# Optimization experiments

Measured on AMD Instinct MI355X. Metric: run time of the kernel, lower is better.

## Reference

```python
import jax, jax.numpy as jnp
import numpy as np
import math

B, N, E, H = 2, 2048, 1024, 16
K = E // H  # head dim = 64


def setup_inputs() -> dict:
    key = jax.random.key(0)
    ks = jax.random.split(key, 9)
    s = 0.02
    return {
        "x": jax.random.normal(ks[0], (B, N, E), jnp.float32),
        "Wq": jax.random.normal(ks[1], (E, E), jnp.float32) * s,
        "bq": jax.random.normal(ks[2], (E,), jnp.float32) * s,
        "Wk": jax.random.normal(ks[3], (E, E), jnp.float32) * s,
        "bk": jax.random.normal(ks[4], (E,), jnp.float32) * s,
        "Wv": jax.random.normal(ks[5], (E, E), jnp.float32) * s,
        "bv": jax.random.normal(ks[6], (E,), jnp.float32) * s,
        "Wp": jax.random.normal(ks[7], (E, E), jnp.float32) * s,
        "bp": jax.random.normal(ks[8], (E,), jnp.float32) * s,
    }


def _split_heads(t):
    # torch: t.transpose(-1,-2).view(b, H, K, N)  -> (B, H, K, N)
    return t.transpose(0, 2, 1).reshape(t.shape[0], H, K, t.shape[1])


def reference(x, Wq, bq, Wk, bk, Wv, bv, Wp, bp):
    b, n, _ = x.shape
    q = _split_heads(x @ Wq.T + bq)  # (B,H,K,N)
    k = _split_heads(x @ Wk.T + bk)
    v = _split_heads(x @ Wv.T + bv)
    # NOTE: module divides by sqrt(query.size(1)) == sqrt(num_heads), not sqrt(head_dim)
    ctx = jnp.einsum('bhkn,bhkm->bhmn', q, k) / math.sqrt(H)  # (B,H,m=key,n=query)
    mask = jnp.triu(jnp.ones((n, n), dtype=bool), 1)  # True where n(query) > m(key)
    ctx = jnp.where(mask[None, None], -jnp.inf, ctx)
    # faithful to source: softmax over last axis (the query axis n)
    ctx = jax.nn.softmax(ctx, axis=-1)
    out = jnp.einsum('bhmn,bhvm->bhvn', ctx, v)  # (B,H,K,N)
    out = out.reshape(b, E, n).transpose(0, 2, 1)  # (B,N,E)
    return out @ Wp.T + bp
```

## Files before the change

### kernel.cpp

```cpp
#include <hip/hip_runtime.h>
#include <hip/hip_bf16.h>

typedef __hip_bfloat16 bf16;
typedef __attribute__((ext_vector_type(8))) short bf16x8;
typedef __attribute__((ext_vector_type(4))) float f32x4;
typedef __attribute__((ext_vector_type(4))) short s16x4;

constexpr int B_ = 2, N_ = 2048, E_ = 1024, H_ = 16, KD_ = 64;
constexpr int M_ = B_ * N_;
constexpr float SCALE = 0.25f * 1.44269504088896f;

#define MFMA16(A, Bf, C) __builtin_amdgcn_mfma_f32_16x16x32_bf16(A, Bf, C, 0, 0, 0)
#define SBAR() do { __builtin_amdgcn_s_barrier(); __builtin_amdgcn_sched_barrier(0); } while (0)
#define WAITCNT(s) asm volatile("s_waitcnt " s ::: "memory")
#define SETPRIO(p) __builtin_amdgcn_s_setprio(p)

typedef const __attribute__((address_space(1))) void* gptr_t;
typedef __attribute__((address_space(3))) void* sptr_t;

__device__ inline short bf16bits(float f) {
  bf16 h = __float2bfloat16(f);
  short s;
  __builtin_memcpy(&s, &h, 2);
  return s;
}
__device__ inline float bf16f(short s) {
  bf16 h;
  __builtin_memcpy(&h, &s, 2);
  return __bfloat162float(h);
}

template <int NROWS, int NTHR>
__device__ inline void stageT(const bf16* __restrict__ base, int stride_elems,
                              char* lds) {
  const int t = threadIdx.x;
#pragma unroll
  for (int i = 0; i < NROWS * 128 / (NTHR * 16); i++) {
    int L = i * NTHR * 16 + t * 16;
    int row = L >> 7;
    int slot = ((L >> 4) & 7) ^ (row & 7);
    const bf16* src = base + (size_t)row * stride_elems + slot * 8;
    __builtin_amdgcn_global_load_lds((gptr_t)(const void*)src,
                                     (sptr_t)(void*)(lds + L), 16, 0, 0);
  }
}

__device__ inline bf16x8 frag_ld(const char* lds, int row, int ks) {
  const int g = (threadIdx.x >> 4) & 3;
  const int off = (ks * 64 + g * 16) ^ ((row & 7) << 4);
  return *(const bf16x8*)(lds + row * 128 + off);
}

__global__ __launch_bounds__(256) void cvt_all(
    const float* __restrict__ x, const float* __restrict__ wq,
    const float* __restrict__ wk, const float* __restrict__ wv,
    const float* __restrict__ wp, bf16* __restrict__ dst) {
  const size_t XN = (size_t)M_ * E_;
  const size_t WN = (size_t)E_ * E_;
  size_t i = ((size_t)blockIdx.x * 256 + threadIdx.x) * 4;
  const float* src;
  size_t off;
  if (i < XN) { src = x; off = i; }
  else if (i < XN + WN) { src = wq; off = i - XN; }
  else if (i < XN + 2 * WN) { src = wk; off = i - XN - WN; }
  else if (i < XN + 3 * WN) { src = wv; off = i - XN - 2 * WN; }
  else { src = wp; off = i - XN - 3 * WN; }
  float4 v = *(const float4*)(src + off);
  s16x4 o;
  o[0] = bf16bits(v.x); o[1] = bf16bits(v.y);
  o[2] = bf16bits(v.z); o[3] = bf16bits(v.w);
  *(s16x4*)(dst + i) = o;
}

__global__ __launch_bounds__(256) void gemm_qkv(
    const bf16* __restrict__ A, const bf16* __restrict__ Wb,
    const float* __restrict__ bq, const float* __restrict__ bk,
    const float* __restrict__ bv, bf16* __restrict__ Qhd,
    bf16* __restrict__ Khd, bf16* __restrict__ Vtd) {
  __shared__ char Asm[16384];
  __shared__ char Bsm[16384];
  const int t = threadIdx.x, lane = t & 63, w = t >> 6;
  const int wr = w >> 1, wc = w & 1;
  const int c = lane & 15, g = lane >> 4;
  const int row0 = blockIdx.y * 128, col0 = blockIdx.x * 128;
  f32x4 acc[4][4] = {};

  for (int k0 = 0; k0 < E_; k0 += 64) {
    stageT<64, 256>(A + (size_t)row0 * E_ + k0, E_, Asm);
    stageT<64, 256>(A + (size_t)(row0 + 64) * E_ + k0, E_, Asm + 8192);
    stageT<64, 256>(Wb + (size_t)col0 * E_ + k0, E_, Bsm);
    stageT<64, 256>(Wb + (size_t)(col0 + 64) * E_ + k0, E_, Bsm + 8192);
    __syncthreads();
#pragma unroll
    for (int ks = 0; ks < 2; ks++) {
      bf16x8 af[4], bfr[4];
#pragma unroll
      for (int mi = 0; mi < 4; mi++) af[mi] = frag_ld(Asm, wr * 64 + mi * 16 + c, ks);
#pragma unroll
      for (int ni = 0; ni < 4; ni++) bfr[ni] = frag_ld(Bsm, wc * 64 + ni * 16 + c, ks);
#pragma unroll
      for (int mi = 0; mi < 4; mi++)
#pragma unroll
        for (int ni = 0; ni < 4; ni++)
          acc[mi][ni] = MFMA16(af[mi], bfr[ni], acc[mi][ni]);
    }
    __syncthreads();
  }

  const int sel = col0 >> 10;
  const float* biasp = sel == 0 ? bq : sel == 1 ? bk : bv;
  bf16* outp = sel == 0 ? Qhd : sel == 1 ? Khd : Vtd;
#pragma unroll
  for (int mi = 0; mi < 4; mi++) {
#pragma unroll
    for (int ni = 0; ni < 4; ni++) {
      const int row = row0 + wr * 64 + mi * 16 + g * 4;
      const int col = col0 + wc * 64 + ni * 16 + c;
      const int ccol = col & 1023, h = ccol >> 6, kd = ccol & 63;
      const float bvf = biasp[ccol];
      if (sel < 2) {
        const float scl = (sel == 1) ? SCALE : 1.0f;
#pragma unroll
        for (int r = 0; r < 4; r++) {
          const int rr = row + r, b = rr >> 11, n = rr & (N_ - 1);
          outp[(((size_t)(b * H_ + h)) * N_ + n) * KD_ + kd] =
              __float2bfloat16((acc[mi][ni][r] + bvf) * scl);
        }
      } else {
        const int b = row >> 11, n = row & (N_ - 1);
        s16x4 o;
#pragma unroll
        for (int r = 0; r < 4; r++) o[r] = bf16bits(acc[mi][ni][r] + bvf);
        *(s16x4*)&outp[(((size_t)(b * H_ + h)) * KD_ + kd) * N_ + n] = o;
      }
    }
  }
}

__global__ __launch_bounds__(256) void gemm_proj(
    const bf16* __restrict__ A, const bf16* __restrict__ Wb,
    const float* __restrict__ bias, float* __restrict__ outf) {
  __shared__ char Asm[16384];
  __shared__ char Bsm[16384];
  const int t = threadIdx.x, lane = t & 63, w = t >> 6;
  const int wr = w >> 1, wc = w & 1;
  const int c = lane & 15, g = lane >> 4;
  const int row0 = blockIdx.y * 128, col0 = blockIdx.x * 128;
  f32x4 acc[4][4] = {};

  for (int k0 = 0; k0 < E_; k0 += 64) {
    stageT<64, 256>(A + (size_t)row0 * E_ + k0, E_, Asm);
    stageT<64, 256>(A + (size_t)(row0 + 64) * E_ + k0, E_, Asm + 8192);
    stageT<64, 256>(Wb + (size_t)col0 * E_ + k0, E_, Bsm);
    stageT<64, 256>(Wb + (size_t)(col0 + 64) * E_ + k0, E_, Bsm + 8192);
    __syncthreads();
#pragma unroll
    for (int ks = 0; ks < 2; ks++) {
      bf16x8 af[4], bfr[4];
#pragma unroll
      for (int mi = 0; mi < 4; mi++) af[mi] = frag_ld(Asm, wr * 64 + mi * 16 + c, ks);
#pragma unroll
      for (int ni = 0; ni < 4; ni++) bfr[ni] = frag_ld(Bsm, wc * 64 + ni * 16 + c, ks);
#pragma unroll
      for (int mi = 0; mi < 4; mi++)
#pragma unroll
        for (int ni = 0; ni < 4; ni++)
          acc[mi][ni] = MFMA16(af[mi], bfr[ni], acc[mi][ni]);
    }
    __syncthreads();
  }

#pragma unroll
  for (int mi = 0; mi < 4; mi++) {
#pragma unroll
    for (int ni = 0; ni < 4; ni++) {
      const int row = row0 + wr * 64 + mi * 16 + g * 4;
      const int col = col0 + wc * 64 + ni * 16 + c;
      const float bvf = bias[col];
#pragma unroll
      for (int r = 0; r < 4; r++)
        outf[(size_t)(row + r) * E_ + col] = acc[mi][ni][r] + bvf;
    }
  }
}

__device__ inline void swz_bid(int& qx, int& bh) {
  const int bid = blockIdx.y * 16 + blockIdx.x;
  const int w = (bid & 7) * 64 + (bid >> 3);
  qx = w & 15;
  bh = w >> 4;
}

__global__ __launch_bounds__(512, 4) void phaseA(
    const bf16* __restrict__ Kh, const bf16* __restrict__ Qh,
    bf16* __restrict__ Vt) {
  __shared__ char Ksm[8192];
  __shared__ char Qsm[2][16384];
  __shared__ float rbuf[2][64];
  const int t = threadIdx.x, lane = t & 63, w = t >> 6;
  const int c = lane & 15, g = (lane >> 4);
  const int wm = w & 3, wn = w >> 2;
  int bx, bh;
  swz_bid(bx, bh);
  const bf16* Kb = Kh + (size_t)bh * N_ * KD_;
  const bf16* Qb = Qh + (size_t)bh * N_ * KD_;
  bf16* Vtb = Vt + (size_t)bh * KD_ * N_;

#pragma unroll 1
  for (int seg = 0; seg < 2; seg++) {
    const int mb = seg ? (31 - bx) : bx;
    const int m0 = mb * 64;
    const int ntE = mb >> 1;

    WAITCNT("lgkmcnt(0)");
    SBAR();
    stageT<64, 512>(Kb + (size_t)m0 * KD_, KD_, Ksm);
    stageT<128, 512>(Qb, KD_, Qsm[0]);
    WAITCNT("vmcnt(2)");
    SBAR();
    bf16x8 af0 = frag_ld(Ksm, wm * 16 + c, 0);
    bf16x8 af1 = frag_ld(Ksm, wm * 16 + c, 1);
    float sm[4] = {};

#pragma unroll 1
    for (int nt = 0; nt <= ntE; nt++) {
      WAITCNT("vmcnt(0) lgkmcnt(0)");
      SBAR();
      if (nt + 1 <= ntE)
        stageT<128, 512>(Qb + (size_t)(nt + 1) * 128 * KD_, KD_,
                         Qsm[(nt + 1) & 1]);
      const char* qs = Qsm[nt & 1];
      if (nt < ntE) {
#pragma unroll
        for (int nf = 0; nf < 4; nf++) {
          const int ni = wn * 4 + nf;
          bf16x8 b0 = frag_ld(qs, ni * 16 + c, 0);
          bf16x8 b1 = frag_ld(qs, ni * 16 + c, 1);
          SETPRIO(1);
          f32x4 sv = {0.f, 0.f, 0.f, 0.f};
          sv = MFMA16(af0, b0, sv);
          sv = MFMA16(af1, b1, sv);
          SETPRIO(0);
#pragma unroll
          for (int r = 0; r < 4; r++) sm[r] += exp2f(sv[r]);
        }
      } else {
        const int mg = m0 + wm * 16 + g * 4;
#pragma unroll
        for (int nf = 0; nf < 4; nf++) {
          const int ni = wn * 4 + nf;
          bf16x8 b0 = frag_ld(qs, ni * 16 + c, 0);
          bf16x8 b1 = frag_ld(qs, ni * 16 + c, 1);
          SETPRIO(1);
          f32x4 sv = {0.f, 0.f, 0.f, 0.f};
          sv = MFMA16(af0, b0, sv);
          sv = MFMA16(af1, b1, sv);
          SETPRIO(0);
          const int ng = nt * 128 + ni * 16 + c;
#pragma unroll
          for (int r = 0; r < 4; r++) {
            float e = exp2f(sv[r]);
            sm[r] += (ng <= mg + r) ? e : 0.f;
          }
        }
      }
    }

#pragma unroll
    for (int r = 0; r < 4; r++) {
      float v = sm[r];
#pragma unroll
      for (int d = 1; d < 16; d <<= 1) v += __shfl_xor(v, d, 64);
      if (c == 0) rbuf[wn][wm * 16 + g * 4 + r] = v;
    }
    WAITCNT("lgkmcnt(0)");
    SBAR();
    {
      const int kd = t >> 3, mc = (t & 7) * 8;
      bf16* p = Vtb + (size_t)kd * N_ + m0 + mc;
      bf16x8 v = *(const bf16x8*)p;
      bf16x8 o;
#pragma unroll
      for (int j = 0; j < 8; j++) {
        const float inv = 1.0f / (rbuf[0][mc + j] + rbuf[1][mc + j]);
        o[j] = bf16bits(bf16f(v[j]) * inv);
      }
      *(bf16x8*)p = o;
    }
  }
}

__global__ __launch_bounds__(512, 4) void phaseB(
    const bf16* __restrict__ Qh, const bf16* __restrict__ Kh,
    const bf16* __restrict__ Vt, bf16* __restrict__ attn) {
  __shared__ char Ksm[2][8192];
  __shared__ char Vsm[2][8192];
  __shared__ char Psm[8192];
  const int t = threadIdx.x, lane = t & 63, w = t >> 6;
  const int c = lane & 15, g = lane >> 4;
  const int wm = w & 3, wn = w >> 2;
  int bx, bh;
  swz_bid(bx, bh);
  const int b = bh >> 4, h = bh & 15;
  const int NT = N_ / 64;
  const bf16* Qb = Qh + (size_t)bh * N_ * KD_;
  const bf16* Kb = Kh + (size_t)bh * N_ * KD_;
  const bf16* Vb = Vt + (size_t)bh * KD_ * N_;

#pragma unroll 1
  for (int seg = 0; seg < 2; seg++) {
    const int qt = seg ? (31 - bx) : bx;
    const int n0 = qt * 64, mt0 = qt;

    WAITCNT("lgkmcnt(0)");
    SBAR();
    stageT<64, 512>(Qb + (size_t)n0 * KD_, KD_, Psm);
    stageT<64, 512>(Kb + (size_t)mt0 * 64 * KD_, KD_, Ksm[mt0 & 1]);
    stageT<64, 512>(Vb + mt0 * 64, N_, Vsm[mt0 & 1]);
    WAITCNT("vmcnt(2)");
    SBAR();
    bf16x8 qf[2][2];
#pragma unroll
    for (int ni = 0; ni < 2; ni++) {
      qf[ni][0] = frag_ld(Psm, wn * 32 + ni * 16 + c, 0);
      qf[ni][1] = frag_ld(Psm, wn * 32 + ni * 16 + c, 1);
    }
    f32x4 out[2] = {};

#pragma unroll 1
    for (int mt = mt0; mt < NT; mt++) {
      WAITCNT("vmcnt(0) lgkmcnt(0)");
      SBAR();
      if (mt + 1 < NT) {
        stageT<64, 512>(Kb + (size_t)(mt + 1) * 64 * KD_, KD_, Ksm[(mt + 1) & 1]);
        stageT<64, 512>(Vb + (mt + 1) * 64, N_, Vsm[(mt + 1) & 1]);
      }
      const char* ksm = Ksm[mt & 1];
      bf16x8 kf0 = frag_ld(ksm, wm * 16 + c, 0);
      bf16x8 kf1 = frag_ld(ksm, wm * 16 + c, 1);
      SETPRIO(1);
      f32x4 sv[2];
#pragma unroll
      for (int ni = 0; ni < 2; ni++) {
        f32x4 z = {0.f, 0.f, 0.f, 0.f};
        z = MFMA16(kf0, qf[ni][0], z);
        z = MFMA16(kf1, qf[ni][1], z);
        sv[ni] = z;
      }
      SETPRIO(0);
      const bool diag = (mt == mt0);
      const int ml = wm * 16 + g * 4;
#pragma unroll
      for (int ni = 0; ni < 2; ni++) {
        const int nl = wn * 32 + ni * 16 + c;
        s16x4 p;
#pragma unroll
        for (int r = 0; r < 4; r++) {
          float val = exp2f(sv[ni][r]);
          if (diag && nl > (ml + r)) val = 0.f;
          p[r] = bf16bits(val);
        }
        const int off = nl * 128 + ((wm * 32 + g * 8) ^ ((nl & 7) << 4));
        *(s16x4*)(Psm + off) = p;
      }
      WAITCNT("lgkmcnt(0)");
      SBAR();
      const char* vsm = Vsm[mt & 1];
      bf16x8 pa0 = frag_ld(Psm, wm * 16 + c, 0);
      bf16x8 pa1 = frag_ld(Psm, wm * 16 + c, 1);
      SETPRIO(1);
#pragma unroll
      for (int ni = 0; ni < 2; ni++) {
        const int kdrow = wn * 32 + ni * 16 + c;
        bf16x8 v0 = frag_ld(vsm, kdrow, 0);
        bf16x8 v1 = frag_ld(vsm, kdrow, 1);
        out[ni] = MFMA16(pa0, v0, out[ni]);
        out[ni] = MFMA16(pa1, v1, out[ni]);
      }
      SETPRIO(0);
    }

#pragma unroll
    for (int ni = 0; ni < 2; ni++) {
#pragma unroll
      for (int r = 0; r < 4; r++) {
        const int n = n0 + wm * 16 + g * 4 + r;
        const int kd = wn * 32 + ni * 16 + c;
        attn[((size_t)(b * N_ + n)) * E_ + h * 64 + kd] =
            __float2bfloat16(out[ni][r]);
      }
    }
  }
}

extern "C" void kernel_launch(void* const* d_in, const int* in_sizes, int n_in,
                              void* d_out, int out_size, void* d_ws, size_t ws_size,
                              hipStream_t stream) {
  (void)in_sizes; (void)n_in; (void)out_size; (void)ws_size;
  const float* x  = (const float*)d_in[0];
  const float* Wq = (const float*)d_in[1];
  const float* bq = (const float*)d_in[2];
  const float* Wk = (const float*)d_in[3];
  const float* bk = (const float*)d_in[4];
  const float* Wv = (const float*)d_in[5];
  const float* bv = (const float*)d_in[6];
  const float* Wp = (const float*)d_in[7];
  const float* bp = (const float*)d_in[8];
  float* out = (float*)d_out;

  const size_t XN = (size_t)M_ * E_;
  const size_t WN = (size_t)E_ * E_;
  const size_t HN = (size_t)B_ * H_ * N_ * KD_;

  bf16* xb   = (bf16*)d_ws;
  bf16* wqkv = xb + XN;
  bf16* wpb  = wqkv + 3 * WN;
  bf16* Qhd  = wpb + WN;
  bf16* Khd  = Qhd + HN;
  bf16* Vtd  = Khd + HN;
  bf16* attn = xb;

  cvt_all<<<dim3(8192), 256, 0, stream>>>(x, Wq, Wk, Wv, Wp, xb);

  gemm_qkv<<<dim3(24, 32), 256, 0, stream>>>(xb, wqkv, bq, bk, bv,
                                             Qhd, Khd, Vtd);

  phaseA<<<dim3(16, B_ * H_), 512, 0, stream>>>(Khd, Qhd, Vtd);
  phaseB<<<dim3(16, B_ * H_), 512, 0, stream>>>(Qhd, Khd, Vtd, attn);

  gemm_proj<<<dim3(8, 32), 256, 0, stream>>>(attn, wpb, bp, out);
}
```

Baseline: 136.2 us.

## Widen attention key tile to 128 to halve loop iterations and barriers

Measured after the change: 137.8 us. About the same (+1.2%).

```diff
diff --git a/kernel.cpp b/kernel.cpp
--- a/kernel.cpp
+++ b/kernel.cpp
@@ -45,10 +45,31 @@
   }
 }
 
+template <int NROWS, int NTHR>
+__device__ inline void stage256(const bf16* __restrict__ base, int stride_elems,
+                                char* lds) {
+  const int t = threadIdx.x;
+#pragma unroll
+  for (int i = 0; i < NROWS * 256 / (NTHR * 16); i++) {
+    int L = i * NTHR * 16 + t * 16;
+    int row = L >> 8;
+    int slot = ((L >> 4) & 15) ^ (row & 15);
+    const bf16* src = base + (size_t)row * stride_elems + slot * 8;
+    __builtin_amdgcn_global_load_lds((gptr_t)(const void*)src,
+                                     (sptr_t)(void*)(lds + L), 16, 0, 0);
+  }
+}
+
 __device__ inline bf16x8 frag_ld(const char* lds, int row, int ks) {
   const int g = (threadIdx.x >> 4) & 3;
   const int off = (ks * 64 + g * 16) ^ ((row & 7) << 4);
   return *(const bf16x8*)(lds + row * 128 + off);
+}
+
+__device__ inline bf16x8 frag_ld256(const char* lds, int row, int ks) {
+  const int g = (threadIdx.x >> 4) & 3;
+  const int off = (ks * 64 + g * 16) ^ ((row & 15) << 4);
+  return *(const bf16x8*)(lds + row * 256 + off);
 }
 
 __global__ __launch_bounds__(256) void cvt_all(
@@ -293,16 +314,15 @@
 __global__ __launch_bounds__(512, 4) void phaseB(
     const bf16* __restrict__ Qh, const bf16* __restrict__ Kh,
     const bf16* __restrict__ Vt, bf16* __restrict__ attn) {
-  __shared__ char Ksm[2][8192];
-  __shared__ char Vsm[2][8192];
-  __shared__ char Psm[8192];
+  __shared__ char Ksm[2][16384];
+  __shared__ char Vsm[2][16384];
+  __shared__ char Psm[16384];
   const int t = threadIdx.x, lane = t & 63, w = t >> 6;
   const int c = lane & 15, g = lane >> 4;
-  const int wm = w & 3, wn = w >> 2;
   int bx, bh;
   swz_bid(bx, bh);
   const int b = bh >> 4, h = bh & 15;
-  const int NT = N_ / 64;
+  const int NT = N_ / 128;
   const bf16* Qb = Qh + (size_t)bh * N_ * KD_;
   const bf16* Kb = Kh + (size_t)bh * N_ * KD_;
   const bf16* Vb = Vt + (size_t)bh * KD_ * N_;
@@ -310,20 +330,20 @@
 #pragma unroll 1
   for (int seg = 0; seg < 2; seg++) {
     const int qt = seg ? (31 - bx) : bx;
-    const int n0 = qt * 64, mt0 = qt;
+    const int n0 = qt * 64, mt0 = qt >> 1;
 
     WAITCNT("lgkmcnt(0)");
     SBAR();
     stageT<64, 512>(Qb + (size_t)n0 * KD_, KD_, Psm);
-    stageT<64, 512>(Kb + (size_t)mt0 * 64 * KD_, KD_, Ksm[mt0 & 1]);
-    stageT<64, 512>(Vb + mt0 * 64, N_, Vsm[mt0 & 1]);
-    WAITCNT("vmcnt(2)");
+    stageT<128, 512>(Kb + (size_t)mt0 * 128 * KD_, KD_, Ksm[mt0 & 1]);
+    stage256<64, 512>(Vb + mt0 * 128, N_, Vsm[mt0 & 1]);
+    WAITCNT("vmcnt(4)");
     SBAR();
-    bf16x8 qf[2][2];
-#pragma unroll
-    for (int ni = 0; ni < 2; ni++) {
-      qf[ni][0] = frag_ld(Psm, wn * 32 + ni * 16 + c, 0);
-      qf[ni][1] = frag_ld(Psm, wn * 32 + ni * 16 + c, 1);
+    bf16x8 qf[4][2];
+#pragma unroll
+    for (int ni = 0; ni < 4; ni++) {
+      qf[ni][0] = frag_ld(Psm, ni * 16 + c, 0);
+      qf[ni][1] = frag_ld(Psm, ni * 16 + c, 1);
     }
     f32x4 out[2] = {};
 
@@ -332,16 +352,17 @@
       WAITCNT("vmcnt(0) lgkmcnt(0)");
       SBAR();
       if (mt + 1 < NT) {
-        stageT<64, 512>(Kb + (size_t)(mt + 1) * 64 * KD_, KD_, Ksm[(mt + 1) & 1]);
-        stageT<64, 512>(Vb + (mt + 1) * 64, N_, Vsm[(mt + 1) & 1]);
+        stageT<128, 512>(Kb + (size_t)(mt + 1) * 128 * KD_, KD_,
+                         Ksm[(mt + 1) & 1]);
+        stage256<64, 512>(Vb + (mt + 1) * 128, N_, Vsm[(mt + 1) & 1]);
       }
       const char* ksm = Ksm[mt & 1];
-      bf16x8 kf0 = frag_ld(ksm, wm * 16 + c, 0);
-      bf16x8 kf1 = frag_ld(ksm, wm * 16 + c, 1);
+      bf16x8 kf0 = frag_ld(ksm, w * 16 + c, 0);
+      bf16x8 kf1 = frag_ld(ksm, w * 16 + c, 1);
       SETPRIO(1);
-      f32x4 sv[2];
-#pragma unroll
-      for (int ni = 0; ni < 2; ni++) {
+      f32x4 sv[4];
+#pragma unroll
+      for (int ni = 0; ni < 4; ni++) {
         f32x4 z = {0.f, 0.f, 0.f, 0.f};
         z = MFMA16(kf0, qf[ni][0], z);
         z = MFMA16(kf1, qf[ni][1], z);
@@ -349,33 +370,37 @@
       }
       SETPRIO(0);
       const bool diag = (mt == mt0);
-      const int ml = wm * 16 + g * 4;
-#pragma unroll
-      for (int ni = 0; ni < 2; ni++) {
-        const int nl = wn * 32 + ni * 16 + c;
+      const int mg = mt * 128 + w * 16 + g * 4;
+#pragma unroll
+      for (int ni = 0; ni < 4; ni++) {
+        const int nl = ni * 16 + c;
+        const int ng = n0 + nl;
         s16x4 p;
 #pragma unroll
         for (int r = 0; r < 4; r++) {
           float val = exp2f(sv[ni][r]);
-          if (diag && nl > (ml + r)) val = 0.f;
+          if (diag && ng > (mg + r)) val = 0.f;
           p[r] = bf16bits(val);
         }
-        const int off = nl * 128 + ((wm * 32 + g * 8) ^ ((nl & 7) << 4));
+        const int off = nl * 256 + ((w * 32 + g * 8) ^ ((nl & 15) << 4));
         *(s16x4*)(Psm + off) = p;
       }
       WAITCNT("lgkmcnt(0)");
       SBAR();
       const char* vsm = Vsm[mt & 1];
-      bf16x8 pa0 = frag_ld(Psm, wm * 16 + c, 0);
-      bf16x8 pa1 = frag_ld(Psm, wm * 16 + c, 1);
+      const int nrow = (w & 3) * 16 + c;
+      bf16x8 pa[4];
+#pragma unroll
+      for (int ks = 0; ks < 4; ks++) pa[ks] = frag_ld256(Psm, nrow, ks);
       SETPRIO(1);
 #pragma unroll
       for (int ni = 0; ni < 2; ni++) {
-        const int kdrow = wn * 32 + ni * 16 + c;
-        bf16x8 v0 = frag_ld(vsm, kdrow, 0);
-        bf16x8 v1 = frag_ld(vsm, kdrow, 1);
-        out[ni] = MFMA16(pa0, v0, out[ni]);
-        out[ni] = MFMA16(pa1, v1, out[ni]);
+        const int kdrow = (w >> 2) * 32 + ni * 16 + c;
+#pragma unroll
+        for (int ks = 0; ks < 4; ks++) {
+          bf16x8 vf = frag_ld256(vsm, kdrow, ks);
+          out[ni] = MFMA16(pa[ks], vf, out[ni]);
+        }
       }
       SETPRIO(0);
     }
@@ -384,8 +409,8 @@
     for (int ni = 0; ni < 2; ni++) {
 #pragma unroll
       for (int r = 0; r < 4; r++) {
-        const int n = n0 + wm * 16 + g * 4 + r;
-        const int kd = wn * 32 + ni * 16 + c;
+        const int n = n0 + (w & 3) * 16 + g * 4 + r;
+        const int kd = (w >> 2) * 32 + ni * 16 + c;
         attn[((size_t)(b * N_ + n)) * E_ + h * 64 + kd] =
             __float2bfloat16(out[ni][r]);
       }
```

## Split phaseB key loop across two parity blocks and merge partial outputs

Applied to the files above, without the earlier changes.

After: 172.9 us. +27.0%, slower.

```diff
diff --git a/kernel.cpp b/kernel.cpp
--- a/kernel.cpp
+++ b/kernel.cpp
@@ -184,13 +184,6 @@
   }
 }
 
-__device__ inline void swz_bid(int& qx, int& bh) {
-  const int bid = blockIdx.y * 16 + blockIdx.x;
-  const int w = (bid & 7) * 64 + (bid >> 3);
-  qx = w & 15;
-  bh = w >> 4;
-}
-
 __global__ __launch_bounds__(512, 4) void phaseA(
     const bf16* __restrict__ Kh, const bf16* __restrict__ Qh,
     bf16* __restrict__ Vt) {
@@ -200,8 +193,9 @@
   const int t = threadIdx.x, lane = t & 63, w = t >> 6;
   const int c = lane & 15, g = (lane >> 4);
   const int wm = w & 3, wn = w >> 2;
-  int bx, bh;
-  swz_bid(bx, bh);
+  const int bid = blockIdx.y * 16 + blockIdx.x;
+  const int ww = (bid & 7) * 64 + (bid >> 3);
+  const int bx = ww & 15, bh = ww >> 4;
   const bf16* Kb = Kh + (size_t)bh * N_ * KD_;
   const bf16* Qb = Qh + (size_t)bh * N_ * KD_;
   bf16* Vtb = Vt + (size_t)bh * KD_ * N_;
@@ -290,33 +284,39 @@
   }
 }
 
-__global__ __launch_bounds__(512, 4) void phaseB(
+__global__ __launch_bounds__(512, 8) void phaseB(
     const bf16* __restrict__ Qh, const bf16* __restrict__ Kh,
-    const bf16* __restrict__ Vt, bf16* __restrict__ attn) {
+    const bf16* __restrict__ Vt, bf16* __restrict__ attn0,
+    bf16* __restrict__ attn1) {
   __shared__ char Ksm[2][8192];
   __shared__ char Vsm[2][8192];
   __shared__ char Psm[8192];
   const int t = threadIdx.x, lane = t & 63, w = t >> 6;
   const int c = lane & 15, g = lane >> 4;
   const int wm = w & 3, wn = w >> 2;
-  int bx, bh;
-  swz_bid(bx, bh);
+  const int bid = blockIdx.y * 64 + blockIdx.x;
+  const int ww = (bid & 7) * 256 + (bid >> 3);
+  const int bh = ww >> 6, qx = (ww >> 1) & 31, p = ww & 1;
   const int b = bh >> 4, h = bh & 15;
   const int NT = N_ / 64;
   const bf16* Qb = Qh + (size_t)bh * N_ * KD_;
   const bf16* Kb = Kh + (size_t)bh * N_ * KD_;
   const bf16* Vb = Vt + (size_t)bh * KD_ * N_;
+  bf16* ap = p ? attn1 : attn0;
 
 #pragma unroll 1
   for (int seg = 0; seg < 2; seg++) {
-    const int qt = seg ? (31 - bx) : bx;
-    const int n0 = qt * 64, mt0 = qt;
+    const int qt = seg ? (31 - qx) : qx;
+    const int n0 = qt * 64;
+    const int mtS = ((qt & 1) == p) ? qt : qt + 1;
 
     WAITCNT("lgkmcnt(0)");
     SBAR();
     stageT<64, 512>(Qb + (size_t)n0 * KD_, KD_, Psm);
-    stageT<64, 512>(Kb + (size_t)mt0 * 64 * KD_, KD_, Ksm[mt0 & 1]);
-    stageT<64, 512>(Vb + mt0 * 64, N_, Vsm[mt0 & 1]);
+    if (mtS < NT) {
+      stageT<64, 512>(Kb + (size_t)mtS * 64 * KD_, KD_, Ksm[(mtS >> 1) & 1]);
+      stageT<64, 512>(Vb + mtS * 64, N_, Vsm[(mtS >> 1) & 1]);
+    }
     WAITCNT("vmcnt(2)");
     SBAR();
     bf16x8 qf[2][2];
@@ -328,14 +328,15 @@
     f32x4 out[2] = {};
 
 #pragma unroll 1
-    for (int mt = mt0; mt < NT; mt++) {
+    for (int mt = mtS; mt < NT; mt += 2) {
       WAITCNT("vmcnt(0) lgkmcnt(0)");
       SBAR();
-      if (mt + 1 < NT) {
-        stageT<64, 512>(Kb + (size_t)(mt + 1) * 64 * KD_, KD_, Ksm[(mt + 1) & 1]);
-        stageT<64, 512>(Vb + (mt + 1) * 64, N_, Vsm[(mt + 1) & 1]);
-      }
-      const char* ksm = Ksm[mt & 1];
+      if (mt + 2 < NT) {
+        stageT<64, 512>(Kb + (size_t)(mt + 2) * 64 * KD_, KD_,
+                        Ksm[((mt + 2) >> 1) & 1]);
+        stageT<64, 512>(Vb + (mt + 2) * 64, N_, Vsm[((mt + 2) >> 1) & 1]);
+      }
+      const char* ksm = Ksm[(mt >> 1) & 1];
       bf16x8 kf0 = frag_ld(ksm, wm * 16 + c, 0);
       bf16x8 kf1 = frag_ld(ksm, wm * 16 + c, 1);
       SETPRIO(1);
@@ -348,24 +349,24 @@
         sv[ni] = z;
       }
       SETPRIO(0);
-      const bool diag = (mt == mt0);
+      const bool diag = (mt == qt);
       const int ml = wm * 16 + g * 4;
 #pragma unroll
       for (int ni = 0; ni < 2; ni++) {
         const int nl = wn * 32 + ni * 16 + c;
-        s16x4 p;
+        s16x4 pk;
 #pragma unroll
         for (int r = 0; r < 4; r++) {
           float val = exp2f(sv[ni][r]);
           if (diag && nl > (ml + r)) val = 0.f;
-          p[r] = bf16bits(val);
+          pk[r] = bf16bits(val);
         }
         const int off = nl * 128 + ((wm * 32 + g * 8) ^ ((nl & 7) << 4));
-        *(s16x4*)(Psm + off) = p;
+        *(s16x4*)(Psm + off) = pk;
       }
       WAITCNT("lgkmcnt(0)");
       SBAR();
-      const char* vsm = Vsm[mt & 1];
+      const char* vsm = Vsm[(mt >> 1) & 1];
       bf16x8 pa0 = frag_ld(Psm, wm * 16 + c, 0);
       bf16x8 pa1 = frag_ld(Psm, wm * 16 + c, 1);
       SETPRIO(1);
@@ -386,11 +387,22 @@
       for (int r = 0; r < 4; r++) {
         const int n = n0 + wm * 16 + g * 4 + r;
         const int kd = wn * 32 + ni * 16 + c;
-        attn[((size_t)(b * N_ + n)) * E_ + h * 64 + kd] =
+        ap[((size_t)(b * N_ + n)) * E_ + h * 64 + kd] =
             __float2bfloat16(out[ni][r]);
       }
     }
   }
+}
+
+__global__ __launch_bounds__(256) void merge_attn(
+    const bf16* __restrict__ a1, bf16* __restrict__ a0) {
+  const size_t i = ((size_t)blockIdx.x * 256 + threadIdx.x) * 8;
+  bf16x8 x0 = *(const bf16x8*)(a0 + i);
+  bf16x8 x1 = *(const bf16x8*)(a1 + i);
+  bf16x8 o;
+#pragma unroll
+  for (int j = 0; j < 8; j++) o[j] = bf16bits(bf16f(x0[j]) + bf16f(x1[j]));
+  *(bf16x8*)(a0 + i) = o;
 }
 
 extern "C" void kernel_launch(void* const* d_in, const int* in_sizes, int n_in,
@@ -412,13 +424,14 @@
   const size_t WN = (size_t)E_ * E_;
   const size_t HN = (size_t)B_ * H_ * N_ * KD_;
 
-  bf16* xb   = (bf16*)d_ws;
-  bf16* wqkv = xb + XN;
-  bf16* wpb  = wqkv + 3 * WN;
-  bf16* Qhd  = wpb + WN;
-  bf16* Khd  = Qhd + HN;
-  bf16* Vtd  = Khd + HN;
-  bf16* attn = xb;
+  bf16* xb    = (bf16*)d_ws;
+  bf16* wqkv  = xb + XN;
+  bf16* wpb   = wqkv + 3 * WN;
+  bf16* Qhd   = wpb + WN;
+  bf16* Khd   = Qhd + HN;
+  bf16* Vtd   = Khd + HN;
+  bf16* attn1 = Vtd + HN;
+  bf16* attn0 = xb;
 
   cvt_all<<<dim3(8192), 256, 0, stream>>>(x, Wq, Wk, Wv, Wp, xb);
 
@@ -426,7 +439,8 @@
                                              Qhd, Khd, Vtd);
 
   phaseA<<<dim3(16, B_ * H_), 512, 0, stream>>>(Khd, Qhd, Vtd);
-  phaseB<<<dim3(16, B_ * H_), 512, 0, stream>>>(Qhd, Khd, Vtd, attn);
-
-  gemm_proj<<<dim3(8, 32), 256, 0, stream>>>(attn, wpb, bp, out);
-}
+  phaseB<<<dim3(64, 32), 512, 0, stream>>>(Qhd, Khd, Vtd, attn0, attn1);
+  merge_attn<<<dim3(2048), 256, 0, stream>>>(attn1, attn0);
+
+  gemm_proj<<<dim3(8, 32), 256, 0, stream>>>(attn0, wpb, bp, out);
+}
```
